# Performance work log

Hardware: AMD Instinct MI355X
Metric: run time of the kernel (lower is better)

The kernel has to match this reference:

```python
import jax, jax.numpy as jnp
import numpy as np

SA_LAMBDA = 1.0
IC_LAMBDA = 1.0
EPS = 1e-12  # torch F.normalize eps


def setup_inputs() -> dict:
    key = jax.random.key(0)
    k1, k2, k3, k4 = jax.random.split(key, 4)
    TF = jax.random.normal(k1, (16, 512, 32, 32), dtype=jnp.float32)
    SF = jax.random.normal(k2, (16, 512, 32, 32), dtype=jnp.float32)
    t_out = jax.random.normal(k3, (16, 21, 128, 128), dtype=jnp.float32)
    s_out = jax.random.normal(k4, (16, 21, 128, 128), dtype=jnp.float32)
    return {"TF": TF, "SF": SF, "t_out": t_out, "s_out": s_out}


def _l2_normalize_last(A):
    # matches torch.nn.functional.normalize(x, dim=2): x / max(||x||, eps)
    n = jnp.linalg.norm(A, axis=-1, keepdims=True)
    return A / jnp.maximum(n, EPS)


def _channel_weighted_spatial_gram(F4):
    # Algebraic fusion of einsum('bij,bki->bijk') + einsum('bijk,bi->bjk'):
    # ATT[b,m,n] = sum_c F[b,c,m] * F[b,c,n] * Fc[b,c]
    b, c, h, w = F4.shape
    Fc = jnp.sum(jnp.abs(F4), axis=(2, 3))          # [b, c]
    Fm = F4.reshape(b, c, h * w)                     # [b, c, M]
    A = jnp.einsum('bcm,bc,bcn->bmn', Fm, Fc, Fm)    # [b, M, M]
    return _l2_normalize_last(A)


def _normalized_channel_gram(L):
    # ICC[b,i,j] = sum_m L[b,i,m] * L[b,j,m], then L2-normalize along last dim
    G = jnp.einsum('bim,bjm->bij', L, L)
    return _l2_normalize_last(G)


def reference(TF, SF, t_out, s_out):
    b, c, h, w = TF.shape
    M = h * w
    ATT_T = _channel_weighted_spatial_gram(TF)
    ATT_S = _channel_weighted_spatial_gram(SF)
    diff = ATT_S - ATT_T
    SA_loss = SA_LAMBDA * jnp.sum(diff * diff) / (b * M ** 2)

    bb, cc, hh, ww = s_out.shape
    s_logit = s_out.reshape(bb, cc, hh * ww)
    t_logit = t_out.reshape(bb, cc, hh * ww)
    G_diff = _normalized_channel_gram(s_logit) - _normalized_channel_gram(t_logit)
    ic_loss = IC_LAMBDA * jnp.sum(G_diff * G_diff) / (cc * bb)

    return (s_out, ic_loss, SA_loss)
```

## Files before the change

kernel.cpp:

```cpp
#include <hip/hip_runtime.h>
#include <hip/hip_bf16.h>
#include <cstdint>
#include <cstddef>

typedef __bf16 bf16x8 __attribute__((ext_vector_type(8)));
typedef float f32x4 __attribute__((ext_vector_type(4)));

__device__ __forceinline__ void gload_lds16(const void* g, void* l) {
  __builtin_amdgcn_global_load_lds((const __attribute__((address_space(1))) void*)g,
                                   (__attribute__((address_space(3))) void*)l, 16, 0, 0);
}

__global__ void __launch_bounds__(256) prep_kernel(const float* __restrict__ TF,
                                                   const float* __restrict__ SF,
                                                   __hip_bfloat16* __restrict__ Wt,
                                                   __hip_bfloat16* __restrict__ Ws) {
  __shared__ float Xs[16 * 1028];
  __shared__ float partial[4][16];
  __shared__ float scale[16];
  int id = blockIdx.x;
  int t = id >> 9, b = (id >> 5) & 15, cb = id & 31;
  const float* Xg = (t ? SF : TF) + ((size_t)b * 512 + (size_t)cb * 16) * 1024;
  __hip_bfloat16* W = (t ? Ws : Wt) + (size_t)b * 524288 + cb * 16;
  int tid = threadIdx.x;
#pragma unroll
  for (int it = 0; it < 16; ++it)
    *reinterpret_cast<float4*>(&Xs[it * 1028 + tid * 4]) =
        *reinterpret_cast<const float4*>(Xg + (size_t)it * 1024 + tid * 4);
  __syncthreads();
  {
    int r = tid & 15, seg = tid >> 4;
    float s = 0.f;
#pragma unroll
    for (int i = 0; i < 16; ++i) {
      float4 v = *reinterpret_cast<const float4*>(&Xs[r * 1028 + seg * 64 + i * 4]);
      s += fabsf(v.x) + fabsf(v.y) + fabsf(v.z) + fabsf(v.w);
    }
    s += __shfl_xor(s, 16); s += __shfl_xor(s, 32);
    if ((tid & 63) < 16) partial[tid >> 6][tid & 15] = s;
    __syncthreads();
    if (tid < 16) scale[tid] = sqrtf(partial[0][tid] + partial[1][tid] + partial[2][tid] + partial[3][tid]);
    __syncthreads();
  }
  float sc[16];
#pragma unroll
  for (int c = 0; c < 16; ++c) sc[c] = scale[c];
#pragma unroll
  for (int j = 0; j < 4; ++j) {
    int m = j * 256 + tid;
    union { __hip_bfloat16 h[16]; uint4 u[2]; } pk;
#pragma unroll
    for (int c = 0; c < 16; ++c) pk.h[c] = __float2bfloat16(Xs[c * 1028 + m] * sc[c]);
    uint4* dst = reinterpret_cast<uint4*>(W + (size_t)m * 512);
    dst[0] = pk.u[0];
    dst[1] = pk.u[1];
  }
}

__device__ __forceinline__ void stage_tile(const __hip_bfloat16* __restrict__ Wm,
                                           const __hip_bfloat16* __restrict__ Wn,
                                           __hip_bfloat16* As, __hip_bfloat16* Bs,
                                           int kt, bool diag) {
  int tid = threadIdx.x, wv = tid >> 6;
#pragma unroll
  for (int i = 0; i < 4; ++i) {
    int ci = i * 256 + tid;
    int row = ci >> 3, slot = ci & 7;
    int gslot = slot ^ (row & 7);
    int wbase = (i * 256 + wv * 64) * 8;
    gload_lds16(Wm + (size_t)row * 512 + kt * 64 + gslot * 8, As + wbase);
    if (!diag)
      gload_lds16(Wn + (size_t)row * 512 + kt * 64 + gslot * 8, Bs + wbase);
  }
}

__global__ void __launch_bounds__(256, 2) syrk_fused_kernel(
    const __hip_bfloat16* __restrict__ Wt, const __hip_bfloat16* __restrict__ Ws,
    float* __restrict__ nT, float* __restrict__ nS, float* __restrict__ cross) {
  __shared__ __hip_bfloat16 As[2][128 * 64], Bs[2][128 * 64];
  int lid = blockIdx.x;
  int swz = (lid & 7) * 72 + (lid >> 3);
  int b = swz / 36, tilec = swz % 36;
  int bx = tilec, tm = 0;
  while (bx >= 8 - tm) { bx -= 8 - tm; ++tm; }
  int tn = tm + bx;
  bool diag = (tm == tn);
  const __hip_bfloat16* WT = Wt + (size_t)b * 524288;
  const __hip_bfloat16* WS = Ws + (size_t)b * 524288;

  const int tid = threadIdx.x;
  const int lane = tid & 63, wv = tid >> 6;
  const int wr = wv >> 1, wc = wv & 1;
  const int g = lane >> 4, c0 = lane & 15;
  const int rx = c0 & 7;

  f32x4 accT[4][4], accS[4][4];
#pragma unroll
  for (int mi = 0; mi < 4; ++mi)
#pragma unroll
    for (int ni = 0; ni < 4; ++ni) {
      accT[mi][ni] = (f32x4){0.f, 0.f, 0.f, 0.f};
      accS[mi][ni] = (f32x4){0.f, 0.f, 0.f, 0.f};
    }

  stage_tile(WT + (size_t)tm * 65536, WT + (size_t)tn * 65536, As[0], Bs[0], 0, diag);
  __syncthreads();

  for (int s = 0; s < 16; ++s) {
    int cur = s & 1;
    if (s < 15) {
      int s1 = s + 1;
      const __hip_bfloat16* base = (s1 < 8) ? WT : WS;
      stage_tile(base + (size_t)tm * 65536, base + (size_t)tn * 65536,
                 As[cur ^ 1], Bs[cur ^ 1], s1 & 7, diag);
    }
    const __hip_bfloat16* Asb = As[cur];
    const __hip_bfloat16* Bsb = diag ? As[cur] : Bs[cur];
    bool isT = (s < 8);
#pragma unroll
    for (int kk = 0; kk < 2; ++kk) {
      int chunk = ((kk * 4 + g) ^ rx) * 8;
      bf16x8 a[4], bb[4];
#pragma unroll
      for (int mi = 0; mi < 4; ++mi)
        a[mi] = *reinterpret_cast<const bf16x8*>(Asb + (wr * 64 + mi * 16 + c0) * 64 + chunk);
#pragma unroll
      for (int ni = 0; ni < 4; ++ni)
        bb[ni] = *reinterpret_cast<const bf16x8*>(Bsb + (wc * 64 + ni * 16 + c0) * 64 + chunk);
      if (isT) {
#pragma unroll
        for (int mi = 0; mi < 4; ++mi)
#pragma unroll
          for (int ni = 0; ni < 4; ++ni)
            accT[mi][ni] = __builtin_amdgcn_mfma_f32_16x16x32_bf16(a[mi], bb[ni], accT[mi][ni], 0, 0, 0);
      } else {
#pragma unroll
        for (int mi = 0; mi < 4; ++mi)
#pragma unroll
          for (int ni = 0; ni < 4; ++ni)
            accS[mi][ni] = __builtin_amdgcn_mfma_f32_16x16x32_bf16(a[mi], bb[ni], accS[mi][ni], 0, 0, 0);
      }
    }
    __syncthreads();
  }

  float* pT = nT + (size_t)b * 1024;
  float* pS = nS + (size_t)b * 1024;
  float* pC = cross + (size_t)b * 1024;
#pragma unroll
  for (int mi = 0; mi < 4; ++mi)
#pragma unroll
    for (int r = 0; r < 4; ++r) {
      float sT = 0.f, sS = 0.f, sC = 0.f;
#pragma unroll
      for (int ni = 0; ni < 4; ++ni) {
        float tv = accT[mi][ni][r], sv = accS[mi][ni][r];
        sT += tv * tv; sS += sv * sv; sC += tv * sv;
      }
#pragma unroll
      for (int msk = 1; msk < 16; msk <<= 1) {
        sT += __shfl_xor(sT, msk); sS += __shfl_xor(sS, msk); sC += __shfl_xor(sC, msk);
      }
      if (c0 == 0) {
        int m = tm * 128 + wr * 64 + mi * 16 + g * 4 + r;
        atomicAdd(pT + m, sT); atomicAdd(pS + m, sS); atomicAdd(pC + m, sC);
      }
    }
  if (!diag) {
#pragma unroll
    for (int ni = 0; ni < 4; ++ni) {
      float sT = 0.f, sS = 0.f, sC = 0.f;
#pragma unroll
      for (int mi = 0; mi < 4; ++mi)
#pragma unroll
        for (int r = 0; r < 4; ++r) {
          float tv = accT[mi][ni][r], sv = accS[mi][ni][r];
          sT += tv * tv; sS += sv * sv; sC += tv * sv;
        }
      sT += __shfl_xor(sT, 16); sS += __shfl_xor(sS, 16); sC += __shfl_xor(sC, 16);
      sT += __shfl_xor(sT, 32); sS += __shfl_xor(sS, 32); sC += __shfl_xor(sC, 32);
      if (g == 0) {
        int n = tn * 128 + wc * 64 + ni * 16 + c0;
        atomicAdd(pT + n, sT); atomicAdd(pS + n, sS); atomicAdd(pC + n, sC);
      }
    }
  }
}

__global__ void icgram2_kernel(const float* __restrict__ t_out, const float* __restrict__ s_out,
                               float* __restrict__ G) {
  __shared__ float lds[22 * 516];
  int chunk = blockIdx.x;
  int z = blockIdx.y;
  int t = z >> 4, bb = z & 15;
  const float* L = (t ? s_out : t_out) + (size_t)bb * 21 * 16384 + (size_t)chunk * 512;
  int tid = threadIdx.x;
  for (int idx = tid; idx < 22 * 128; idx += 264) {
    int r = idx >> 7, c = idx & 127;
    float4 v;
    if (r < 21) v = *reinterpret_cast<const float4*>(L + (size_t)r * 16384 + c * 4);
    else { v.x = 0.f; v.y = 0.f; v.z = 0.f; v.w = 0.f; }
    *reinterpret_cast<float4*>(&lds[r * 516 + c * 4]) = v;
  }
  __syncthreads();
  int ms = tid & 3, pb = tid >> 2;
  int p = pb, gi = 0;
  while (p >= 11 - gi) { p -= 11 - gi; gi++; }
  int gj = gi + p;
  const float* ri0 = &lds[(2 * gi) * 516 + ms * 128];
  const float* ri1 = ri0 + 516;
  const float* rj0 = &lds[(2 * gj) * 516 + ms * 128];
  const float* rj1 = rj0 + 516;
  float a00 = 0.f, a01 = 0.f, a10 = 0.f, a11 = 0.f;
#pragma unroll
  for (int mi = 0; mi < 32; ++mi) {
    float4 va0 = *reinterpret_cast<const float4*>(ri0 + mi * 4);
    float4 va1 = *reinterpret_cast<const float4*>(ri1 + mi * 4);
    float4 vb0 = *reinterpret_cast<const float4*>(rj0 + mi * 4);
    float4 vb1 = *reinterpret_cast<const float4*>(rj1 + mi * 4);
    a00 += va0.x * vb0.x + va0.y * vb0.y + va0.z * vb0.z + va0.w * vb0.w;
    a01 += va0.x * vb1.x + va0.y * vb1.y + va0.z * vb1.z + va0.w * vb1.w;
    a10 += va1.x * vb0.x + va1.y * vb0.y + va1.z * vb0.z + va1.w * vb0.w;
    a11 += va1.x * vb1.x + va1.y * vb1.y + va1.z * vb1.z + va1.w * vb1.w;
  }
  a00 += __shfl_xor(a00, 1); a00 += __shfl_xor(a00, 2);
  a01 += __shfl_xor(a01, 1); a01 += __shfl_xor(a01, 2);
  a10 += __shfl_xor(a10, 1); a10 += __shfl_xor(a10, 2);
  a11 += __shfl_xor(a11, 1); a11 += __shfl_xor(a11, 2);
  if (ms == 0) {
    float* Gz = G + (size_t)z * 441;
    int i0 = 2 * gi, i1 = i0 + 1, j0 = 2 * gj, j1 = j0 + 1;
    atomicAdd(&Gz[i0 * 21 + j0], a00);
    if (j1 < 21) atomicAdd(&Gz[i0 * 21 + j1], a01);
    if (i1 < 21 && gi != gj) atomicAdd(&Gz[i1 * 21 + j0], a10);
    if (i1 < 21 && j1 < 21) atomicAdd(&Gz[i1 * 21 + j1], a11);
  }
}

__global__ void finalize_kernel(const float* __restrict__ G, const float* __restrict__ nT,
                                const float* __restrict__ nS, const float* __restrict__ cross,
                                float* __restrict__ out2) {
  __shared__ float red[16];
  int tid = threadIdx.x;
  float sa = 0.f;
#pragma unroll
  for (int it = 0; it < 4; ++it) {
    int i4 = it * 1024 + tid;
    float4 a = reinterpret_cast<const float4*>(nT)[i4];
    float4 s4 = reinterpret_cast<const float4*>(nS)[i4];
    float4 c4 = reinterpret_cast<const float4*>(cross)[i4];
#pragma unroll
    for (int k = 0; k < 4; ++k) {
      float a1 = (&a.x)[k], s1 = (&s4.x)[k], c1 = (&c4.x)[k];
      float NT = fmaxf(sqrtf(a1), 1e-12f), NS = fmaxf(sqrtf(s1), 1e-12f);
      sa += a1 / (NT * NT) + s1 / (NS * NS) - 2.f * c1 / (NT * NS);
    }
  }
  float ic = 0.f;
  if (tid < 336) {
    int b = tid / 21, i = tid % 21;
    const float* gt = G + (size_t)b * 441;
    const float* gs = G + (size_t)(16 + b) * 441;
    float nt = 0.f, ns = 0.f;
    for (int j = 0; j < 21; ++j) {
      int idx2 = (i <= j) ? i * 21 + j : j * 21 + i;
      float vt = gt[idx2], vs = gs[idx2];
      nt += vt * vt; ns += vs * vs;
    }
    float rt = 1.f / fmaxf(sqrtf(nt), 1e-12f);
    float rs = 1.f / fmaxf(sqrtf(ns), 1e-12f);
    for (int j = 0; j < 21; ++j) {
      int idx2 = (i <= j) ? i * 21 + j : j * 21 + i;
      float d = gs[idx2] * rs - gt[idx2] * rt;
      ic += d * d;
    }
  }
  int lane = tid & 63, wv = tid >> 6;
#pragma unroll
  for (int m = 32; m; m >>= 1) { sa += __shfl_xor(sa, m); ic += __shfl_xor(ic, m); }
  if (lane == 0) red[wv] = sa;
  __syncthreads();
  if (tid == 0) { float s = 0.f; for (int w = 0; w < 16; ++w) s += red[w]; out2[1] = s * (1.0f / 16777216.0f); }
  __syncthreads();
  if (lane == 0) red[wv] = ic;
  __syncthreads();
  if (tid == 0) { float s = 0.f; for (int w = 0; w < 16; ++w) s += red[w]; out2[0] = s * (1.0f / 336.0f); }
}

extern "C" void kernel_launch(void* const* d_in, const int* in_sizes, int n_in,
                              void* d_out, int out_size, void* d_ws, size_t ws_size,
                              hipStream_t stream) {
  const float* TF = (const float*)d_in[0];
  const float* SF = (const float*)d_in[1];
  const float* t_out = (const float*)d_in[2];
  const float* s_out = (const float*)d_in[3];
  float* out = (float*)d_out;
  char* ws = (char*)d_ws;

  float* nT = (float*)(ws + 0);
  float* nS = (float*)(ws + 65536);
  float* cross = (float*)(ws + 131072);
  float* G = (float*)(ws + 196608);
  __hip_bfloat16* Wt = (__hip_bfloat16*)(ws + 262144);
  __hip_bfloat16* Ws = (__hip_bfloat16*)(ws + 262144 + 16777216);

  hipMemcpyAsync(d_out, (const void*)s_out, (size_t)5505024 * 4, hipMemcpyDeviceToDevice, stream);
  hipMemsetAsync(ws, 0, 253056, stream);

  prep_kernel<<<1024, 256, 0, stream>>>(TF, SF, Wt, Ws);
  syrk_fused_kernel<<<576, 256, 0, stream>>>(Wt, Ws, nT, nS, cross);
  icgram2_kernel<<<dim3(32, 32), 264, 0, stream>>>(t_out, s_out, G);
  finalize_kernel<<<1, 1024, 0, stream>>>(G, nT, nS, cross, out + 5505024);
}
```

Measured before the change: 125.8 us.

## Split SYRK tiles for more blocks, fuse output copy into icgram, bf16 prep LDS

The SYRK kernel now gives each 128x128 tile pair to two blocks, each covering half the N columns. It uses a K step of 32 with smaller LDS buffers and a higher occupancy hint, so 1152 blocks run instead of 576. The separate device-to-device copy of s_out is removed; the icgram kernel writes s_out rows into the output while it loads them. The prep kernel stores the staged data as bf16 in LDS and computes the channel abs-sums on the fly, dropping one LDS pass. The trade-offs are more global reads of the A tiles, twice as many atomics, and rounding to bf16 before the scale is applied, which adds a second rounding step.

Result: slower. 150.0 us (+19.3%).

```diff
diff --git a/kernel.cpp b/kernel.cpp
--- a/kernel.cpp
+++ b/kernel.cpp
@@ -11,135 +11,133 @@
                                    (__attribute__((address_space(3))) void*)l, 16, 0, 0);
 }
 
+__device__ __forceinline__ unsigned short f2bf(float x) {
+  return __builtin_bit_cast(unsigned short, __float2bfloat16(x));
+}
+
 __global__ void __launch_bounds__(256) prep_kernel(const float* __restrict__ TF,
                                                    const float* __restrict__ SF,
                                                    __hip_bfloat16* __restrict__ Wt,
                                                    __hip_bfloat16* __restrict__ Ws) {
-  __shared__ float Xs[16 * 1028];
-  __shared__ float partial[4][16];
+  __shared__ __hip_bfloat16 Xs[16 * 1040];
   __shared__ float scale[16];
   int id = blockIdx.x;
   int t = id >> 9, b = (id >> 5) & 15, cb = id & 31;
   const float* Xg = (t ? SF : TF) + ((size_t)b * 512 + (size_t)cb * 16) * 1024;
   __hip_bfloat16* W = (t ? Ws : Wt) + (size_t)b * 524288 + cb * 16;
   int tid = threadIdx.x;
-#pragma unroll
-  for (int it = 0; it < 16; ++it)
-    *reinterpret_cast<float4*>(&Xs[it * 1028 + tid * 4]) =
-        *reinterpret_cast<const float4*>(Xg + (size_t)it * 1024 + tid * 4);
-  __syncthreads();
-  {
-    int r = tid & 15, seg = tid >> 4;
-    float s = 0.f;
-#pragma unroll
-    for (int i = 0; i < 16; ++i) {
-      float4 v = *reinterpret_cast<const float4*>(&Xs[r * 1028 + seg * 64 + i * 4]);
-      s += fabsf(v.x) + fabsf(v.y) + fabsf(v.z) + fabsf(v.w);
-    }
-    s += __shfl_xor(s, 16); s += __shfl_xor(s, 32);
-    if ((tid & 63) < 16) partial[tid >> 6][tid & 15] = s;
-    __syncthreads();
-    if (tid < 16) scale[tid] = sqrtf(partial[0][tid] + partial[1][tid] + partial[2][tid] + partial[3][tid]);
-    __syncthreads();
-  }
+  int ch = tid >> 4, seg = tid & 15;
+  const float* rowp = Xg + (size_t)ch * 1024 + seg * 64;
+  float s = 0.f;
+#pragma unroll
+  for (int i = 0; i < 16; ++i) {
+    float4 v = *reinterpret_cast<const float4*>(rowp + i * 4);
+    s += fabsf(v.x) + fabsf(v.y) + fabsf(v.z) + fabsf(v.w);
+    ushort4 hv;
+    hv.x = f2bf(v.x); hv.y = f2bf(v.y);
+    hv.z = f2bf(v.z); hv.w = f2bf(v.w);
+    *reinterpret_cast<ushort4*>(&Xs[ch * 1040 + seg * 64 + i * 4]) = hv;
+  }
+  s += __shfl_xor(s, 1); s += __shfl_xor(s, 2);
+  s += __shfl_xor(s, 4); s += __shfl_xor(s, 8);
+  if (seg == 0) scale[ch] = sqrtf(s);
+  __syncthreads();
   float sc[16];
 #pragma unroll
   for (int c = 0; c < 16; ++c) sc[c] = scale[c];
 #pragma unroll
   for (int j = 0; j < 4; ++j) {
     int m = j * 256 + tid;
-    union { __hip_bfloat16 h[16]; uint4 u[2]; } pk;
-#pragma unroll
-    for (int c = 0; c < 16; ++c) pk.h[c] = __float2bfloat16(Xs[c * 1028 + m] * sc[c]);
+    union { unsigned short h[16]; uint4 u[2]; } pk;
+#pragma unroll
+    for (int c = 0; c < 16; ++c)
+      pk.h[c] = f2bf(__bfloat162float(Xs[c * 1040 + m]) * sc[c]);
     uint4* dst = reinterpret_cast<uint4*>(W + (size_t)m * 512);
     dst[0] = pk.u[0];
     dst[1] = pk.u[1];
   }
 }
 
-__device__ __forceinline__ void stage_tile(const __hip_bfloat16* __restrict__ Wm,
-                                           const __hip_bfloat16* __restrict__ Wn,
-                                           __hip_bfloat16* As, __hip_bfloat16* Bs,
-                                           int kt, bool diag) {
-  int tid = threadIdx.x, wv = tid >> 6;
-#pragma unroll
-  for (int i = 0; i < 4; ++i) {
-    int ci = i * 256 + tid;
-    int row = ci >> 3, slot = ci & 7;
-    int gslot = slot ^ (row & 7);
-    int wbase = (i * 256 + wv * 64) * 8;
-    gload_lds16(Wm + (size_t)row * 512 + kt * 64 + gslot * 8, As + wbase);
-    if (!diag)
-      gload_lds16(Wn + (size_t)row * 512 + kt * 64 + gslot * 8, Bs + wbase);
-  }
-}
-
-__global__ void __launch_bounds__(256, 2) syrk_fused_kernel(
+__global__ void __launch_bounds__(256, 4) syrk_fused_kernel(
     const __hip_bfloat16* __restrict__ Wt, const __hip_bfloat16* __restrict__ Ws,
     float* __restrict__ nT, float* __restrict__ nS, float* __restrict__ cross) {
-  __shared__ __hip_bfloat16 As[2][128 * 64], Bs[2][128 * 64];
-  int lid = blockIdx.x;
-  int swz = (lid & 7) * 72 + (lid >> 3);
-  int b = swz / 36, tilec = swz % 36;
-  int bx = tilec, tm = 0;
+  __shared__ __hip_bfloat16 As2[2][128 * 32];
+  __shared__ __hip_bfloat16 Bs2[2][64 * 32];
+  int bid = blockIdx.x;
+  int j = (bid & 7) * 144 + (bid >> 3);
+  int b = j / 72, r72 = j % 72;
+  int p = r72 >> 1, h = r72 & 1;
+  int bx = p, tm = 0;
   while (bx >= 8 - tm) { bx -= 8 - tm; ++tm; }
   int tn = tm + bx;
   bool diag = (tm == tn);
-  const __hip_bfloat16* WT = Wt + (size_t)b * 524288;
-  const __hip_bfloat16* WS = Ws + (size_t)b * 524288;
+  const __hip_bfloat16* WTb = Wt + (size_t)b * 524288;
+  const __hip_bfloat16* WSb = Ws + (size_t)b * 524288;
+  const __hip_bfloat16* At = WTb + (size_t)tm * 65536;
+  const __hip_bfloat16* Asrc = WSb + (size_t)tm * 65536;
+  const __hip_bfloat16* Btg = WTb + (size_t)(tn * 128 + h * 64) * 512;
+  const __hip_bfloat16* Bsg = WSb + (size_t)(tn * 128 + h * 64) * 512;
 
   const int tid = threadIdx.x;
   const int lane = tid & 63, wv = tid >> 6;
   const int wr = wv >> 1, wc = wv & 1;
   const int g = lane >> 4, c0 = lane & 15;
-  const int rx = c0 & 7;
-
-  f32x4 accT[4][4], accS[4][4];
+  const int kc = (g ^ ((c0 >> 1) & 3)) * 8;
+
+  f32x4 accT[4][2], accS[4][2];
 #pragma unroll
   for (int mi = 0; mi < 4; ++mi)
 #pragma unroll
-    for (int ni = 0; ni < 4; ++ni) {
+    for (int ni = 0; ni < 2; ++ni) {
       accT[mi][ni] = (f32x4){0.f, 0.f, 0.f, 0.f};
       accS[mi][ni] = (f32x4){0.f, 0.f, 0.f, 0.f};
     }
 
-  stage_tile(WT + (size_t)tm * 65536, WT + (size_t)tn * 65536, As[0], Bs[0], 0, diag);
-  __syncthreads();
-
-  for (int s = 0; s < 16; ++s) {
+  auto stage = [&](int s, int buf) {
+    int kt = (s & 15) * 32;
+    const __hip_bfloat16* Ab = (s < 16) ? At : Asrc;
+#pragma unroll
+    for (int i = 0; i < 2; ++i) {
+      int ci = i * 256 + tid;
+      int row = ci >> 2, slot = ci & 3;
+      int gs = slot ^ ((row >> 1) & 3);
+      gload_lds16(Ab + (size_t)row * 512 + kt + gs * 8, &As2[buf][(i * 256 + wv * 64) * 8]);
+    }
+    if (!diag) {
+      const __hip_bfloat16* Bb = (s < 16) ? Btg : Bsg;
+      int row = tid >> 2, slot = tid & 3;
+      int gs = slot ^ ((row >> 1) & 3);
+      gload_lds16(Bb + (size_t)row * 512 + kt + gs * 8, &Bs2[buf][(wv * 64) * 8]);
+    }
+  };
+
+  stage(0, 0);
+  __syncthreads();
+
+  for (int s = 0; s < 32; ++s) {
     int cur = s & 1;
-    if (s < 15) {
-      int s1 = s + 1;
-      const __hip_bfloat16* base = (s1 < 8) ? WT : WS;
-      stage_tile(base + (size_t)tm * 65536, base + (size_t)tn * 65536,
-                 As[cur ^ 1], Bs[cur ^ 1], s1 & 7, diag);
-    }
-    const __hip_bfloat16* Asb = As[cur];
-    const __hip_bfloat16* Bsb = diag ? As[cur] : Bs[cur];
-    bool isT = (s < 8);
-#pragma unroll
-    for (int kk = 0; kk < 2; ++kk) {
-      int chunk = ((kk * 4 + g) ^ rx) * 8;
-      bf16x8 a[4], bb[4];
+    if (s < 31) stage(s + 1, cur ^ 1);
+    const __hip_bfloat16* Asb = As2[cur];
+    const __hip_bfloat16* Bsb = diag ? (As2[cur] + h * 64 * 32) : Bs2[cur];
+    bf16x8 a[4], bb[2];
+#pragma unroll
+    for (int mi = 0; mi < 4; ++mi)
+      a[mi] = *reinterpret_cast<const bf16x8*>(Asb + (wr * 64 + mi * 16 + c0) * 32 + kc);
+#pragma unroll
+    for (int ni = 0; ni < 2; ++ni)
+      bb[ni] = *reinterpret_cast<const bf16x8*>(Bsb + (wc * 32 + ni * 16 + c0) * 32 + kc);
+    if (s < 16) {
 #pragma unroll
       for (int mi = 0; mi < 4; ++mi)
-        a[mi] = *reinterpret_cast<const bf16x8*>(Asb + (wr * 64 + mi * 16 + c0) * 64 + chunk);
-#pragma unroll
-      for (int ni = 0; ni < 4; ++ni)
-        bb[ni] = *reinterpret_cast<const bf16x8*>(Bsb + (wc * 64 + ni * 16 + c0) * 64 + chunk);
-      if (isT) {
-#pragma unroll
-        for (int mi = 0; mi < 4; ++mi)
-#pragma unroll
-          for (int ni = 0; ni < 4; ++ni)
-            accT[mi][ni] = __builtin_amdgcn_mfma_f32_16x16x32_bf16(a[mi], bb[ni], accT[mi][ni], 0, 0, 0);
-      } else {
-#pragma unroll
-        for (int mi = 0; mi < 4; ++mi)
-#pragma unroll
-          for (int ni = 0; ni < 4; ++ni)
-            accS[mi][ni] = __builtin_amdgcn_mfma_f32_16x16x32_bf16(a[mi], bb[ni], accS[mi][ni], 0, 0, 0);
-      }
+#pragma unroll
+        for (int ni = 0; ni < 2; ++ni)
+          accT[mi][ni] = __builtin_amdgcn_mfma_f32_16x16x32_bf16(a[mi], bb[ni], accT[mi][ni], 0, 0, 0);
+    } else {
+#pragma unroll
+      for (int mi = 0; mi < 4; ++mi)
+#pragma unroll
+        for (int ni = 0; ni < 2; ++ni)
+          accS[mi][ni] = __builtin_amdgcn_mfma_f32_16x16x32_bf16(a[mi], bb[ni], accS[mi][ni], 0, 0, 0);
     }
     __syncthreads();
   }
@@ -153,7 +151,7 @@
     for (int r = 0; r < 4; ++r) {
       float sT = 0.f, sS = 0.f, sC = 0.f;
 #pragma unroll
-      for (int ni = 0; ni < 4; ++ni) {
+      for (int ni = 0; ni < 2; ++ni) {
         float tv = accT[mi][ni][r], sv = accS[mi][ni][r];
         sT += tv * tv; sS += sv * sv; sC += tv * sv;
       }
@@ -168,7 +166,7 @@
     }
   if (!diag) {
 #pragma unroll
-    for (int ni = 0; ni < 4; ++ni) {
+    for (int ni = 0; ni < 2; ++ni) {
       float sT = 0.f, sS = 0.f, sC = 0.f;
 #pragma unroll
       for (int mi = 0; mi < 4; ++mi)
@@ -180,60 +178,67 @@
       sT += __shfl_xor(sT, 16); sS += __shfl_xor(sS, 16); sC += __shfl_xor(sC, 16);
       sT += __shfl_xor(sT, 32); sS += __shfl_xor(sS, 32); sC += __shfl_xor(sC, 32);
       if (g == 0) {
-        int n = tn * 128 + wc * 64 + ni * 16 + c0;
+        int n = tn * 128 + h * 64 + wc * 32 + ni * 16 + c0;
         atomicAdd(pT + n, sT); atomicAdd(pS + n, sS); atomicAdd(pC + n, sC);
       }
     }
   }
 }
 
-__global__ void icgram2_kernel(const float* __restrict__ t_out, const float* __restrict__ s_out,
-                               float* __restrict__ G) {
+__global__ void __launch_bounds__(256) icgram2_kernel(const float* __restrict__ t_out,
+                                                      const float* __restrict__ s_out,
+                                                      float* __restrict__ G,
+                                                      float* __restrict__ outcpy) {
   __shared__ float lds[22 * 516];
   int chunk = blockIdx.x;
   int z = blockIdx.y;
   int t = z >> 4, bb = z & 15;
-  const float* L = (t ? s_out : t_out) + (size_t)bb * 21 * 16384 + (size_t)chunk * 512;
+  const float* L = (t ? s_out : t_out) + (size_t)bb * 344064 + (size_t)chunk * 512;
+  float* O = outcpy + (size_t)bb * 344064 + (size_t)chunk * 512;
   int tid = threadIdx.x;
-  for (int idx = tid; idx < 22 * 128; idx += 264) {
+  for (int idx = tid; idx < 22 * 128; idx += 256) {
     int r = idx >> 7, c = idx & 127;
     float4 v;
-    if (r < 21) v = *reinterpret_cast<const float4*>(L + (size_t)r * 16384 + c * 4);
-    else { v.x = 0.f; v.y = 0.f; v.z = 0.f; v.w = 0.f; }
+    if (r < 21) {
+      v = *reinterpret_cast<const float4*>(L + (size_t)r * 16384 + c * 4);
+      if (t) *reinterpret_cast<float4*>(O + (size_t)r * 16384 + c * 4) = v;
+    } else { v.x = 0.f; v.y = 0.f; v.z = 0.f; v.w = 0.f; }
     *reinterpret_cast<float4*>(&lds[r * 516 + c * 4]) = v;
   }
   __syncthreads();
-  int ms = tid & 3, pb = tid >> 2;
-  int p = pb, gi = 0;
-  while (p >= 11 - gi) { p -= 11 - gi; gi++; }
-  int gj = gi + p;
-  const float* ri0 = &lds[(2 * gi) * 516 + ms * 128];
-  const float* ri1 = ri0 + 516;
-  const float* rj0 = &lds[(2 * gj) * 516 + ms * 128];
-  const float* rj1 = rj0 + 516;
-  float a00 = 0.f, a01 = 0.f, a10 = 0.f, a11 = 0.f;
-#pragma unroll
-  for (int mi = 0; mi < 32; ++mi) {
-    float4 va0 = *reinterpret_cast<const float4*>(ri0 + mi * 4);
-    float4 va1 = *reinterpret_cast<const float4*>(ri1 + mi * 4);
-    float4 vb0 = *reinterpret_cast<const float4*>(rj0 + mi * 4);
-    float4 vb1 = *reinterpret_cast<const float4*>(rj1 + mi * 4);
-    a00 += va0.x * vb0.x + va0.y * vb0.y + va0.z * vb0.z + va0.w * vb0.w;
-    a01 += va0.x * vb1.x + va0.y * vb1.y + va0.z * vb1.z + va0.w * vb1.w;
-    a10 += va1.x * vb0.x + va1.y * vb0.y + va1.z * vb0.z + va1.w * vb0.w;
-    a11 += va1.x * vb1.x + va1.y * vb1.y + va1.z * vb1.z + va1.w * vb1.w;
-  }
-  a00 += __shfl_xor(a00, 1); a00 += __shfl_xor(a00, 2);
-  a01 += __shfl_xor(a01, 1); a01 += __shfl_xor(a01, 2);
-  a10 += __shfl_xor(a10, 1); a10 += __shfl_xor(a10, 2);
-  a11 += __shfl_xor(a11, 1); a11 += __shfl_xor(a11, 2);
-  if (ms == 0) {
-    float* Gz = G + (size_t)z * 441;
-    int i0 = 2 * gi, i1 = i0 + 1, j0 = 2 * gj, j1 = j0 + 1;
-    atomicAdd(&Gz[i0 * 21 + j0], a00);
-    if (j1 < 21) atomicAdd(&Gz[i0 * 21 + j1], a01);
-    if (i1 < 21 && gi != gj) atomicAdd(&Gz[i1 * 21 + j0], a10);
-    if (i1 < 21 && j1 < 21) atomicAdd(&Gz[i1 * 21 + j1], a11);
+  int ms = tid & 3;
+  for (int pb = tid >> 2; pb < 66; pb += 64) {
+    int pp = pb, gi = 0;
+    while (pp >= 11 - gi) { pp -= 11 - gi; gi++; }
+    int gj = gi + pp;
+    const float* ri0 = &lds[(2 * gi) * 516 + ms * 128];
+    const float* ri1 = ri0 + 516;
+    const float* rj0 = &lds[(2 * gj) * 516 + ms * 128];
+    const float* rj1 = rj0 + 516;
+    float a00 = 0.f, a01 = 0.f, a10 = 0.f, a11 = 0.f;
+#pragma unroll
+    for (int mi = 0; mi < 32; ++mi) {
+      float4 va0 = *reinterpret_cast<const float4*>(ri0 + mi * 4);
+      float4 va1 = *reinterpret_cast<const float4*>(ri1 + mi * 4);
+      float4 vb0 = *reinterpret_cast<const float4*>(rj0 + mi * 4);
+      float4 vb1 = *reinterpret_cast<const float4*>(rj1 + mi * 4);
+      a00 += va0.x * vb0.x + va0.y * vb0.y + va0.z * vb0.z + va0.w * vb0.w;
+      a01 += va0.x * vb1.x + va0.y * vb1.y + va0.z * vb1.z + va0.w * vb1.w;
+      a10 += va1.x * vb0.x + va1.y * vb0.y + va1.z * vb0.z + va1.w * vb0.w;
+      a11 += va1.x * vb1.x + va1.y * vb1.y + va1.z * vb1.z + va1.w * vb1.w;
+    }
+    a00 += __shfl_xor(a00, 1); a00 += __shfl_xor(a00, 2);
+    a01 += __shfl_xor(a01, 1); a01 += __shfl_xor(a01, 2);
+    a10 += __shfl_xor(a10, 1); a10 += __shfl_xor(a10, 2);
+    a11 += __shfl_xor(a11, 1); a11 += __shfl_xor(a11, 2);
+    if (ms == 0) {
+      float* Gz = G + (size_t)z * 441;
+      int i0 = 2 * gi, i1 = i0 + 1, j0 = 2 * gj, j1 = j0 + 1;
+      atomicAdd(&Gz[i0 * 21 + j0], a00);
+      if (j1 < 21) atomicAdd(&Gz[i0 * 21 + j1], a01);
+      if (i1 < 21 && gi != gj) atomicAdd(&Gz[i1 * 21 + j0], a10);
+      if (i1 < 21 && j1 < 21) atomicAdd(&Gz[i1 * 21 + j1], a11);
+    }
   }
 }
 
@@ -304,11 +309,10 @@
   __hip_bfloat16* Wt = (__hip_bfloat16*)(ws + 262144);
   __hip_bfloat16* Ws = (__hip_bfloat16*)(ws + 262144 + 16777216);
 
-  hipMemcpyAsync(d_out, (const void*)s_out, (size_t)5505024 * 4, hipMemcpyDeviceToDevice, stream);
-  hipMemsetAsync(ws, 0, 253056, stream);
+  (void)hipMemsetAsync(ws, 0, 253056, stream);
 
   prep_kernel<<<1024, 256, 0, stream>>>(TF, SF, Wt, Ws);
-  syrk_fused_kernel<<<576, 256, 0, stream>>>(Wt, Ws, nT, nS, cross);
-  icgram2_kernel<<<dim3(32, 32), 264, 0, stream>>>(t_out, s_out, G);
+  syrk_fused_kernel<<<1152, 256, 0, stream>>>(Wt, Ws, nT, nS, cross);
+  icgram2_kernel<<<dim3(32, 32), 256, 0, stream>>>(t_out, s_out, G, out);
   finalize_kernel<<<1, 1024, 0, stream>>>(G, nT, nS, cross, out + 5505024);
 }
```
